# Kernel tuning notes

Hardware: AMD Instinct MI355X
Metric: run time of the kernel (lower is better)

Reference implementation:

```python
import jax, jax.numpy as jnp
import numpy as np
import math

DIM = 768
HEADS = 12
HEAD_DIM = DIM // HEADS
EPS = 1e-6


def rms_norm(x, w):
    return x * jax.lax.rsqrt(jnp.mean(x * x, axis=-1, keepdims=True) + EPS) * w


def rotate_half(x):
    # torch.cat([-x[..., 1::2], x[..., ::2]], dim=-1)
    return jnp.concatenate([-x[..., 1::2], x[..., ::2]], axis=-1)


def setup_inputs() -> dict:
    key = jax.random.key(0)
    ks = jax.random.split(key, 12)
    b, n = 2, 2048
    s = 0.02
    return {
        "x": jax.random.normal(ks[0], (b, n, DIM), jnp.float32),
        "cos": jax.random.uniform(ks[1], (1, 1, n, HEAD_DIM), jnp.float32),
        "sin": jax.random.uniform(ks[2], (1, 1, n, HEAD_DIM), jnp.float32),
        "mask": jnp.zeros((1, 1, n, n), jnp.float32),
        "wq": jax.random.normal(ks[3], (DIM, DIM), jnp.float32) * s,
        "wk": jax.random.normal(ks[4], (DIM, DIM), jnp.float32) * s,
        "wv": jax.random.normal(ks[5], (DIM, DIM), jnp.float32) * s,
        "wo": jax.random.normal(ks[6], (DIM, DIM), jnp.float32) * s,
        "bo": jnp.zeros((DIM,), jnp.float32),
        "g_attn": jnp.ones((DIM,), jnp.float32),
        "g_ffn": jnp.ones((DIM,), jnp.float32),
        "w1": jax.random.normal(ks[7], (DIM, 4 * DIM), jnp.float32) * s,
        "b1": jnp.zeros((4 * DIM,), jnp.float32),
        "w2": jax.random.normal(ks[8], (4 * DIM, DIM), jnp.float32) * s,
        "b2": jnp.zeros((DIM,), jnp.float32),
    }


def reference(x, cos, sin, mask, wq, wk, wv, wo, bo, g_attn, g_ffn, w1, b1, w2, b2):
    b, n, _ = x.shape
    h = rms_norm(x, g_attn)
    # [b, n, dim] -> [b, heads, n, head_dim]
    def split_heads(t):
        return t.reshape(b, n, HEADS, HEAD_DIM).transpose(0, 2, 1, 3)
    q = split_heads(h @ wq)
    k = split_heads(h @ wk)
    v = split_heads(h @ wv)
    q = q * cos + rotate_half(q) * sin
    k = k * cos + rotate_half(k) * sin
    scores = jnp.einsum("bhqd,bhkd->bhqk", q, k) / math.sqrt(HEAD_DIM)
    scores = scores + mask
    attn = jax.nn.softmax(scores, axis=-1)
    out = jnp.einsum("bhqk,bhkd->bhqd", attn, v)
    out = out.transpose(0, 2, 1, 3).reshape(b, n, DIM)
    x = x + (out @ wo + bo)  # dropout is identity in eval
    h2 = rms_norm(x, g_ffn)
    ffn = jax.nn.silu(h2 @ w1 + b1) @ w2 + b2
    return x + ffn
```

## Files before the change

### kernel.cpp

```cpp
#include <hip/hip_runtime.h>
#include <hip/hip_bf16.h>

typedef unsigned short u16;
typedef unsigned int u32;
typedef float f32x4 __attribute__((ext_vector_type(4)));
typedef short bf16x8 __attribute__((ext_vector_type(8)));
typedef int i32x4 __attribute__((ext_vector_type(4)));
typedef unsigned short u16x8 __attribute__((ext_vector_type(8)));

#define DIM 768
#define NTOK 4096
#define NSEQ 2048
#define NHEAD 12
#define HDIM 64

__device__ __forceinline__ u16 f2bf(float f) {
    u32 u = __builtin_bit_cast(u32, f);
    u32 r = (u + 0x7FFFu + ((u >> 16) & 1u)) >> 16;
    return (u16)r;
}
__device__ __forceinline__ float bf2f(u16 h) {
    return __builtin_bit_cast(float, ((u32)h) << 16);
}

__global__ __launch_bounds__(256) void rmsnorm_cast(
    const float* __restrict__ X, const float* __restrict__ g, u16* __restrict__ H)
{
    const int row = blockIdx.x;
    const int tid = threadIdx.x;
    const float* xr = X + (long)row * DIM;
    float v0 = xr[tid], v1 = xr[tid + 256], v2 = xr[tid + 512];
    float ss = v0 * v0 + v1 * v1 + v2 * v2;
    #pragma unroll
    for (int o = 1; o < 64; o <<= 1) ss += __shfl_xor(ss, o);
    __shared__ float wsum[4];
    if ((tid & 63) == 0) wsum[tid >> 6] = ss;
    __syncthreads();
    float tot = wsum[0] + wsum[1] + wsum[2] + wsum[3];
    float sc = rsqrtf(tot * (1.0f / DIM) + 1e-6f);
    u16* hr = H + (long)row * DIM;
    hr[tid]       = f2bf(v0 * sc * g[tid]);
    hr[tid + 256] = f2bf(v1 * sc * g[tid + 256]);
    hr[tid + 512] = f2bf(v2 * sc * g[tid + 512]);
}

__global__ __launch_bounds__(256) void transpose_cvt(
    const float* __restrict__ in, u16* __restrict__ out, int R, int C)
{
    __shared__ float t[64][65];
    const int tid = threadIdx.x;
    const long ct = (long)blockIdx.x * 64, rt = (long)blockIdx.y * 64;
    #pragma unroll
    for (int j = 0; j < 4; ++j) {
        int f = j * 256 + tid;
        int row = f >> 4, c0 = (f & 15) * 4;
        f32x4 v = *(const f32x4*)(in + (rt + row) * C + ct + c0);
        #pragma unroll
        for (int i = 0; i < 4; ++i) t[row][c0 + i] = v[i];
    }
    __syncthreads();
    #pragma unroll
    for (int j = 0; j < 2; ++j) {
        int f = j * 256 + tid;
        int c = f >> 3, r0 = (f & 7) * 8;
        u16x8 o;
        #pragma unroll
        for (int i = 0; i < 8; ++i) o[i] = f2bf(t[r0 + i][c]);
        *(u16x8*)(out + (ct + c) * R + rt + r0) = o;
    }
}

__device__ __forceinline__ void rope_row(const u16* __restrict__ src,
                                         u16* __restrict__ dst,
                                         const float* __restrict__ cs,
                                         const float* __restrict__ sn)
{
    u16x8 qv[8];
    #pragma unroll
    for (int i = 0; i < 8; ++i) qv[i] = ((const u16x8*)src)[i];
    u16x8 ov[8];
    #pragma unroll
    for (int j = 0; j < 32; ++j) {
        float xj  = bf2f(qv[j >> 3][j & 7]);
        float xo  = bf2f(qv[(2 * j + 1) >> 3][(2 * j + 1) & 7]);
        float xhj = bf2f(qv[(32 + j) >> 3][j & 7]);
        float xe  = bf2f(qv[(2 * j) >> 3][(2 * j) & 7]);
        float lo = xj * cs[j] - xo * sn[j];
        float hi = xhj * cs[32 + j] + xe * sn[32 + j];
        ov[j >> 3][j & 7] = f2bf(lo);
        ov[4 + (j >> 3)][j & 7] = f2bf(hi);
    }
    #pragma unroll
    for (int i = 0; i < 8; ++i) ((u16x8*)dst)[i] = ov[i];
}

__global__ __launch_bounds__(256) void rope_qk(
    const u16* __restrict__ QKV, const float* __restrict__ cosT,
    const float* __restrict__ sinT, u16* __restrict__ Qr, u16* __restrict__ Kr)
{
    int gid = blockIdx.x * 256 + threadIdx.x;
    int h = gid % NHEAD, token = gid / NHEAD;
    int b = token >> 11, n = token & 2047;
    const float* cs = cosT + (long)n * HDIM;
    const float* sn = sinT + (long)n * HDIM;
    long dsto = (((long)b * NHEAD + h) * NSEQ + n) * HDIM;
    rope_row(QKV + (long)token * 2304 + h * HDIM,       Qr + dsto, cs, sn);
    rope_row(QKV + (long)token * 2304 + DIM + h * HDIM, Kr + dsto, cs, sn);
}

__global__ __launch_bounds__(256) void v_transpose(
    const u16* __restrict__ QKV, u16* __restrict__ Vt)
{
    __shared__ u32 t[64][65];
    const int tid = threadIdx.x;
    const int nt = blockIdx.x, bh = blockIdx.y;
    const int b = bh / NHEAD, h = bh - b * NHEAD;
    const long tok0 = (long)b * NSEQ + nt * 64;
    #pragma unroll
    for (int j = 0; j < 2; ++j) {
        int f = j * 256 + tid;
        int n = f >> 3, d0 = (f & 7) * 8;
        u16x8 v = *(const u16x8*)(QKV + (tok0 + n) * 2304 + 1536 + h * HDIM + d0);
        #pragma unroll
        for (int i = 0; i < 8; ++i) t[n][d0 + i] = v[i];
    }
    __syncthreads();
    #pragma unroll
    for (int j = 0; j < 2; ++j) {
        int f = j * 256 + tid;
        int d = f >> 3, n0 = (f & 7) * 8;
        u16x8 o;
        #pragma unroll
        for (int i = 0; i < 8; ++i) o[i] = (u16)t[n0 + i][d];
        *(u16x8*)(Vt + ((long)bh * HDIM + d) * NSEQ + nt * 64 + n0) = o;
    }
}

template <int EPI>
__global__ __launch_bounds__(256) void gemm_nt(
    const u16* __restrict__ A, const u16* __restrict__ Bt,
    void* __restrict__ Cp, const float* __restrict__ bias,
    const float* __restrict__ resid, int M, int N, int K, int ldc)
{
    __shared__ __align__(16) char smA[128 * 128];
    __shared__ __align__(16) char smB[128 * 128];
    const int tid = threadIdx.x, lane = tid & 63, wid = tid >> 6;
    const int wr = wid >> 1, wc = wid & 1;
    const long mbase = (long)blockIdx.y * 128, nbase = (long)blockIdx.x * 128;
    const char* Ab = (const char*)A;
    const char* Bb = (const char*)Bt;
    const long strideA = (long)K * 2;

    i32x4 pa[4], pb[4];
    auto loadTile = [&](int kt) {
        long k0b = (long)kt * 128;
        #pragma unroll
        for (int j = 0; j < 4; ++j) {
            int f = (j * 256 + tid) * 16;
            int row = f >> 7, kb = f & 127;
            pa[j] = *(const i32x4*)(Ab + (mbase + row) * strideA + k0b + kb);
            pb[j] = *(const i32x4*)(Bb + (nbase + row) * strideA + k0b + kb);
        }
    };
    auto writeTile = [&]() {
        #pragma unroll
        for (int j = 0; j < 4; ++j) {
            int f = (j * 256 + tid) * 16;
            int row = f >> 7, kb = f & 127;
            int sw = kb ^ ((row & 7) << 4);
            *(i32x4*)(smA + row * 128 + sw) = pa[j];
            *(i32x4*)(smB + row * 128 + sw) = pb[j];
        }
    };

    const f32x4 zero4 = {0.f, 0.f, 0.f, 0.f};
    f32x4 acc[4][4];
    #pragma unroll
    for (int m = 0; m < 4; ++m)
        #pragma unroll
        for (int n = 0; n < 4; ++n) acc[m][n] = zero4;

    const int KT = K >> 6;
    loadTile(0);
    for (int kt = 0; kt < KT; ++kt) {
        __syncthreads();
        writeTile();
        __syncthreads();
        if (kt + 1 < KT) loadTile(kt + 1);
        #pragma unroll
        for (int ks = 0; ks < 2; ++ks) {
            const int kbyte = ks * 64 + ((lane >> 4) << 4);
            bf16x8 af[4], bfr[4];
            #pragma unroll
            for (int m = 0; m < 4; ++m) {
                int row = wr * 64 + m * 16 + (lane & 15);
                af[m] = *(const bf16x8*)(smA + row * 128 + (kbyte ^ ((row & 7) << 4)));
            }
            #pragma unroll
            for (int n = 0; n < 4; ++n) {
                int row = wc * 64 + n * 16 + (lane & 15);
                bfr[n] = *(const bf16x8*)(smB + row * 128 + (kbyte ^ ((row & 7) << 4)));
            }
            #pragma unroll
            for (int m = 0; m < 4; ++m)
                #pragma unroll
                for (int n = 0; n < 4; ++n)
                    acc[m][n] = __builtin_amdgcn_mfma_f32_16x16x32_bf16(
                        af[m], bfr[n], acc[m][n], 0, 0, 0);
        }
    }

    #pragma unroll
    for (int m = 0; m < 4; ++m)
        #pragma unroll
        for (int n = 0; n < 4; ++n)
            #pragma unroll
            for (int r = 0; r < 4; ++r) {
                long row = mbase + wr * 64 + m * 16 + ((lane >> 4) << 2) + r;
                long col = nbase + wc * 64 + n * 16 + (lane & 15);
                long idx = row * ldc + col;
                float v = acc[m][n][r];
                if (EPI == 0) {
                    ((u16*)Cp)[idx] = f2bf(v);
                } else if (EPI == 1) {
                    ((float*)Cp)[idx] = resid[idx] + v + bias[col];
                } else {
                    float t = v + bias[col];
                    ((u16*)Cp)[idx] = f2bf(t / (1.0f + __expf(-t)));
                }
            }
}

__global__ __launch_bounds__(256) void attn_fwd(
    const u16* __restrict__ Qr, const u16* __restrict__ Kr,
    const u16* __restrict__ Vt, u16* __restrict__ AO)
{
    __shared__ __align__(16) char smQ[128 * 128];
    __shared__ __align__(16) char smK[64 * 128];
    __shared__ __align__(16) char smV[64 * 128];
    __shared__ __align__(16) char smP[4 * 32 * 128];
    const int tid = threadIdx.x, lane = tid & 63, wid = tid >> 6;
    const int qt = blockIdx.x, bh = blockIdx.y;
    const char* Qg = (const char*)(Qr + ((long)bh * NSEQ + qt * 128) * HDIM);
    const char* Kg = (const char*)(Kr + (long)bh * NSEQ * HDIM);
    const char* Vg = (const char*)(Vt + (long)bh * HDIM * NSEQ);

    #pragma unroll
    for (int j = 0; j < 4; ++j) {
        int f = (j * 256 + tid) * 16;
        int row = f >> 7, kb = f & 127;
        i32x4 v = *(const i32x4*)(Qg + row * 128 + kb);
        *(i32x4*)(smQ + row * 128 + (kb ^ ((row & 7) << 4))) = v;
    }
    __syncthreads();
    bf16x8 qf[2][2];
    #pragma unroll
    for (int mq = 0; mq < 2; ++mq)
        #pragma unroll
        for (int ks = 0; ks < 2; ++ks) {
            int row = wid * 32 + mq * 16 + (lane & 15);
            int kbyte = ks * 64 + ((lane >> 4) << 4);
            qf[mq][ks] = *(const bf16x8*)(smQ + row * 128 + (kbyte ^ ((row & 7) << 4)));
        }

    const f32x4 zero4 = {0.f, 0.f, 0.f, 0.f};
    f32x4 oacc[2][4];
    float mst[2][4], lst[2][4];
    #pragma unroll
    for (int mq = 0; mq < 2; ++mq) {
        #pragma unroll
        for (int df = 0; df < 4; ++df) oacc[mq][df] = zero4;
        #pragma unroll
        for (int r = 0; r < 4; ++r) { mst[mq][r] = -1e30f; lst[mq][r] = 0.f; }
    }

    i32x4 pk[2], pv[2];
    auto loadKV = [&](int kb) {
        #pragma unroll
        for (int j = 0; j < 2; ++j) {
            int f = (j * 256 + tid) * 16;
            int row = f >> 7, c = f & 127;
            pk[j] = *(const i32x4*)(Kg + ((long)kb * 64 + row) * 128 + c);
            pv[j] = *(const i32x4*)(Vg + (long)row * (NSEQ * 2) + kb * 128 + c);
        }
    };
    loadKV(0);

    for (int kb = 0; kb < 32; ++kb) {
        __syncthreads();
        #pragma unroll
        for (int j = 0; j < 2; ++j) {
            int f = (j * 256 + tid) * 16;
            int row = f >> 7, c = f & 127;
            int sw = c ^ ((row & 7) << 4);
            *(i32x4*)(smK + row * 128 + sw) = pk[j];
            *(i32x4*)(smV + row * 128 + sw) = pv[j];
        }
        __syncthreads();
        if (kb + 1 < 32) loadKV(kb + 1);

        f32x4 s[2][4];
        #pragma unroll
        for (int mq = 0; mq < 2; ++mq)
            #pragma unroll
            for (int n = 0; n < 4; ++n) s[mq][n] = zero4;
        #pragma unroll
        for (int ks = 0; ks < 2; ++ks) {
            int kbyte = ks * 64 + ((lane >> 4) << 4);
            bf16x8 kf[4];
            #pragma unroll
            for (int n = 0; n < 4; ++n) {
                int row = n * 16 + (lane & 15);
                kf[n] = *(const bf16x8*)(smK + row * 128 + (kbyte ^ ((row & 7) << 4)));
            }
            #pragma unroll
            for (int mq = 0; mq < 2; ++mq)
                #pragma unroll
                for (int n = 0; n < 4; ++n)
                    s[mq][n] = __builtin_amdgcn_mfma_f32_16x16x32_bf16(
                        qf[mq][ks], kf[n], s[mq][n], 0, 0, 0);
        }

        #pragma unroll
        for (int mq = 0; mq < 2; ++mq) {
            float rmax[4] = {-1e30f, -1e30f, -1e30f, -1e30f};
            #pragma unroll
            for (int n = 0; n < 4; ++n)
                #pragma unroll
                for (int r = 0; r < 4; ++r) {
                    s[mq][n][r] *= 0.125f;
                    rmax[r] = fmaxf(rmax[r], s[mq][n][r]);
                }
            #pragma unroll
            for (int o = 1; o < 16; o <<= 1)
                #pragma unroll
                for (int r = 0; r < 4; ++r)
                    rmax[r] = fmaxf(rmax[r], __shfl_xor(rmax[r], o));
            float corr[4], rsum[4] = {0.f, 0.f, 0.f, 0.f};
            #pragma unroll
            for (int r = 0; r < 4; ++r) {
                float mnew = fmaxf(mst[mq][r], rmax[r]);
                corr[r] = __expf(mst[mq][r] - mnew);
                mst[mq][r] = mnew;
            }
            #pragma unroll
            for (int n = 0; n < 4; ++n)
                #pragma unroll
                for (int r = 0; r < 4; ++r) {
                    float p = __expf(s[mq][n][r] - mst[mq][r]);
                    s[mq][n][r] = p;
                    rsum[r] += p;
                }
            #pragma unroll
            for (int o = 1; o < 16; o <<= 1)
                #pragma unroll
                for (int r = 0; r < 4; ++r) rsum[r] += __shfl_xor(rsum[r], o);
            #pragma unroll
            for (int r = 0; r < 4; ++r) lst[mq][r] = lst[mq][r] * corr[r] + rsum[r];
            #pragma unroll
            for (int df = 0; df < 4; ++df)
                #pragma unroll
                for (int r = 0; r < 4; ++r) oacc[mq][df][r] *= corr[r];
            #pragma unroll
            for (int n = 0; n < 4; ++n)
                #pragma unroll
                for (int r = 0; r < 4; ++r) {
                    int row = wid * 32 + mq * 16 + ((lane >> 4) << 2) + r;
                    int colb = (n * 16 + (lane & 15)) * 2;
                    *(u16*)(smP + row * 128 + (colb ^ ((row & 7) << 4))) =
                        f2bf(s[mq][n][r]);
                }
        }

        #pragma unroll
        for (int ks = 0; ks < 2; ++ks) {
            int kbyte = ks * 64 + ((lane >> 4) << 4);
            bf16x8 vf[4];
            #pragma unroll
            for (int df = 0; df < 4; ++df) {
                int row = df * 16 + (lane & 15);
                vf[df] = *(const bf16x8*)(smV + row * 128 + (kbyte ^ ((row & 7) << 4)));
            }
            #pragma unroll
            for (int mq = 0; mq < 2; ++mq) {
                int rowp = wid * 32 + mq * 16 + (lane & 15);
                bf16x8 pf = *(const bf16x8*)(smP + rowp * 128 + (kbyte ^ ((rowp & 7) << 4)));
                #pragma unroll
                for (int df = 0; df < 4; ++df)
                    oacc[mq][df] = __builtin_amdgcn_mfma_f32_16x16x32_bf16(
                        pf, vf[df], oacc[mq][df], 0, 0, 0);
            }
        }
    }

    const int b = bh / NHEAD, h = bh - b * NHEAD;
    #pragma unroll
    for (int mq = 0; mq < 2; ++mq)
        #pragma unroll
        for (int df = 0; df < 4; ++df)
            #pragma unroll
            for (int r = 0; r < 4; ++r) {
                long token = (long)b * NSEQ + qt * 128 + wid * 32 + mq * 16 +
                             ((lane >> 4) << 2) + r;
                int col = h * HDIM + df * 16 + (lane & 15);
                AO[token * DIM + col] = f2bf(oacc[mq][df][r] / lst[mq][r]);
            }
}

extern "C" void kernel_launch(void* const* d_in, const int* in_sizes, int n_in,
                              void* d_out, int out_size, void* d_ws, size_t ws_size,
                              hipStream_t stream) {
    const float* x      = (const float*)d_in[0];
    const float* cosT   = (const float*)d_in[1];
    const float* sinT   = (const float*)d_in[2];
    const float* wq     = (const float*)d_in[4];
    const float* wk     = (const float*)d_in[5];
    const float* wv     = (const float*)d_in[6];
    const float* wo     = (const float*)d_in[7];
    const float* bo     = (const float*)d_in[8];
    const float* g_attn = (const float*)d_in[9];
    const float* g_ffn  = (const float*)d_in[10];
    const float* w1     = (const float*)d_in[11];
    const float* b1     = (const float*)d_in[12];
    const float* w2     = (const float*)d_in[13];
    const float* b2     = (const float*)d_in[14];
    float* out = (float*)d_out;
    char* ws = (char*)d_ws;

    constexpr long SZ_H    = (long)NTOK * DIM * 2;
    constexpr long SZ_WQKV = 2304L * DIM * 2;
    constexpr long SZ_WO   = (long)DIM * DIM * 2;
    constexpr long SZ_W1   = 3072L * DIM * 2;
    constexpr long SZ_W2   = (long)DIM * 3072 * 2;
    constexpr long SZ_QKV  = (long)NTOK * 2304 * 2;
    constexpr long SZ_QR   = 24L * NSEQ * HDIM * 2;
    constexpr long SZ_AO   = (long)NTOK * DIM * 2;

    const long OFF_H    = 0;
    const long OFF_WQKV = OFF_H + SZ_H;
    const long OFF_WO   = OFF_WQKV + SZ_WQKV;
    const long OFF_W1   = OFF_WO + SZ_WO;
    const long OFF_W2   = OFF_W1 + SZ_W1;
    const long OFF_QKV  = OFF_W2 + SZ_W2;
    const long OFF_QR   = OFF_QKV + SZ_QKV;
    const long OFF_KR   = OFF_QR + SZ_QR;
    const long OFF_VT   = OFF_KR + SZ_QR;
    const long OFF_AO   = OFF_VT + SZ_QR;
    const long OFF_X2   = OFF_AO + SZ_AO;
    const long OFF_FFN1 = OFF_QKV;

    u16* H     = (u16*)(ws + OFF_H);
    u16* WQKVT = (u16*)(ws + OFF_WQKV);
    u16* WOT   = (u16*)(ws + OFF_WO);
    u16* W1T   = (u16*)(ws + OFF_W1);
    u16* W2T   = (u16*)(ws + OFF_W2);
    u16* QKV   = (u16*)(ws + OFF_QKV);
    u16* QR    = (u16*)(ws + OFF_QR);
    u16* KR    = (u16*)(ws + OFF_KR);
    u16* VT    = (u16*)(ws + OFF_VT);
    u16* AO    = (u16*)(ws + OFF_AO);
    float* X2  = (float*)(ws + OFF_X2);
    u16* FFN1  = (u16*)(ws + OFF_FFN1);

    transpose_cvt<<<dim3(12, 12), 256, 0, stream>>>(wq, WQKVT,                 DIM, DIM);
    transpose_cvt<<<dim3(12, 12), 256, 0, stream>>>(wk, WQKVT + 768L * 768,    DIM, DIM);
    transpose_cvt<<<dim3(12, 12), 256, 0, stream>>>(wv, WQKVT + 2L * 768 * 768, DIM, DIM);
    transpose_cvt<<<dim3(12, 12), 256, 0, stream>>>(wo, WOT, DIM, DIM);
    transpose_cvt<<<dim3(48, 12), 256, 0, stream>>>(w1, W1T, DIM, 3072);
    transpose_cvt<<<dim3(12, 48), 256, 0, stream>>>(w2, W2T, 3072, DIM);

    rmsnorm_cast<<<NTOK, 256, 0, stream>>>(x, g_attn, H);
    gemm_nt<0><<<dim3(18, 32), 256, 0, stream>>>(H, WQKVT, QKV, nullptr, nullptr,
                                                 NTOK, 2304, DIM, 2304);
    rope_qk<<<192, 256, 0, stream>>>(QKV, cosT, sinT, QR, KR);
    v_transpose<<<dim3(32, 24), 256, 0, stream>>>(QKV, VT);
    attn_fwd<<<dim3(16, 24), 256, 0, stream>>>(QR, KR, VT, AO);
    gemm_nt<1><<<dim3(6, 32), 256, 0, stream>>>(AO, WOT, X2, bo, x,
                                                NTOK, DIM, DIM, DIM);

    rmsnorm_cast<<<NTOK, 256, 0, stream>>>(X2, g_ffn, H);
    gemm_nt<2><<<dim3(24, 32), 256, 0, stream>>>(H, W1T, FFN1, b1, nullptr,
                                                 NTOK, 3072, DIM, 3072);
    gemm_nt<1><<<dim3(6, 32), 256, 0, stream>>>(FFN1, W2T, out, b2, X2,
                                                NTOK, DIM, 3072, DIM);
}
```

Measured before the change: 367.0 us.

## Use direct global-to-LDS loads in GEMM and attention, shrink attention query tile

GEMM and attention now stage tiles with global_load_lds, writing straight into shared memory with pre-swizzled source addresses, instead of going through registers. This drops the register prefetch, so the load of the next tile no longer overlaps compute, and each iteration waits on a barrier. Attention blocks now cover 64 queries instead of 128 (one 16-row MFMA tile per wave), which doubles the grid for more parallelism but means K/V is reloaded twice as often. The four 768x768 weight transposes are merged into a single launch.

```diff
diff --git a/kernel.cpp b/kernel.cpp
--- a/kernel.cpp
+++ b/kernel.cpp
@@ -21,6 +21,12 @@
 }
 __device__ __forceinline__ float bf2f(u16 h) {
     return __builtin_bit_cast(float, ((u32)h) << 16);
+}
+
+__device__ __forceinline__ void gload16(const void* g, void* l) {
+    __builtin_amdgcn_global_load_lds(
+        (const __attribute__((address_space(1))) unsigned int*)g,
+        (__attribute__((address_space(3))) unsigned int*)l, 16, 0, 0);
 }
 
 __global__ __launch_bounds__(256) void rmsnorm_cast(
@@ -44,12 +50,12 @@
     hr[tid + 512] = f2bf(v2 * sc * g[tid + 512]);
 }
 
-__global__ __launch_bounds__(256) void transpose_cvt(
-    const float* __restrict__ in, u16* __restrict__ out, int R, int C)
+__device__ __forceinline__ void transpose_cvt_body(
+    const float* __restrict__ in, u16* __restrict__ out, int R, int C,
+    int bx, int by, int tid)
 {
     __shared__ float t[64][65];
-    const int tid = threadIdx.x;
-    const long ct = (long)blockIdx.x * 64, rt = (long)blockIdx.y * 64;
+    const long ct = (long)bx * 64, rt = (long)by * 64;
     #pragma unroll
     for (int j = 0; j < 4; ++j) {
         int f = j * 256 + tid;
@@ -68,6 +74,28 @@
         for (int i = 0; i < 8; ++i) o[i] = f2bf(t[r0 + i][c]);
         *(u16x8*)(out + (ct + c) * R + rt + r0) = o;
     }
+}
+
+__global__ __launch_bounds__(256) void transpose_cvt(
+    const float* __restrict__ in, u16* __restrict__ out, int R, int C)
+{
+    transpose_cvt_body(in, out, R, C, blockIdx.x, blockIdx.y, threadIdx.x);
+}
+
+struct Cvt4Args {
+    const float* in0; const float* in1; const float* in2; const float* in3;
+    u16* out0; u16* out1; u16* out2; u16* out3;
+};
+__global__ __launch_bounds__(256) void transpose_cvt4(Cvt4Args a)
+{
+    const float* in; u16* out;
+    switch (blockIdx.z) {
+        case 0: in = a.in0; out = a.out0; break;
+        case 1: in = a.in1; out = a.out1; break;
+        case 2: in = a.in2; out = a.out2; break;
+        default: in = a.in3; out = a.out3; break;
+    }
+    transpose_cvt_body(in, out, DIM, DIM, blockIdx.x, blockIdx.y, threadIdx.x);
 }
 
 __device__ __forceinline__ void rope_row(const u16* __restrict__ src,
@@ -151,28 +179,6 @@
     const char* Bb = (const char*)Bt;
     const long strideA = (long)K * 2;
 
-    i32x4 pa[4], pb[4];
-    auto loadTile = [&](int kt) {
-        long k0b = (long)kt * 128;
-        #pragma unroll
-        for (int j = 0; j < 4; ++j) {
-            int f = (j * 256 + tid) * 16;
-            int row = f >> 7, kb = f & 127;
-            pa[j] = *(const i32x4*)(Ab + (mbase + row) * strideA + k0b + kb);
-            pb[j] = *(const i32x4*)(Bb + (nbase + row) * strideA + k0b + kb);
-        }
-    };
-    auto writeTile = [&]() {
-        #pragma unroll
-        for (int j = 0; j < 4; ++j) {
-            int f = (j * 256 + tid) * 16;
-            int row = f >> 7, kb = f & 127;
-            int sw = kb ^ ((row & 7) << 4);
-            *(i32x4*)(smA + row * 128 + sw) = pa[j];
-            *(i32x4*)(smB + row * 128 + sw) = pb[j];
-        }
-    };
-
     const f32x4 zero4 = {0.f, 0.f, 0.f, 0.f};
     f32x4 acc[4][4];
     #pragma unroll
@@ -181,12 +187,18 @@
         for (int n = 0; n < 4; ++n) acc[m][n] = zero4;
 
     const int KT = K >> 6;
-    loadTile(0);
     for (int kt = 0; kt < KT; ++kt) {
+        const long k0b = (long)kt * 128;
+        #pragma unroll
+        for (int j = 0; j < 4; ++j) {
+            int flat = (j * 256 + tid) * 16;
+            int row = flat >> 7, c = flat & 127;
+            int csw = c ^ ((row & 7) << 4);
+            int ldst = (j * 256 + (tid & 192)) * 16;
+            gload16(Ab + (mbase + row) * strideA + k0b + csw, smA + ldst);
+            gload16(Bb + (nbase + row) * strideA + k0b + csw, smB + ldst);
+        }
         __syncthreads();
-        writeTile();
-        __syncthreads();
-        if (kt + 1 < KT) loadTile(kt + 1);
         #pragma unroll
         for (int ks = 0; ks < 2; ++ks) {
             const int kbyte = ks * 64 + ((lane >> 4) << 4);
@@ -208,6 +220,7 @@
                     acc[m][n] = __builtin_amdgcn_mfma_f32_16x16x32_bf16(
                         af[m], bfr[n], acc[m][n], 0, 0, 0);
         }
+        __syncthreads();
     }
 
     #pragma unroll
@@ -235,75 +248,55 @@
     const u16* __restrict__ Qr, const u16* __restrict__ Kr,
     const u16* __restrict__ Vt, u16* __restrict__ AO)
 {
-    __shared__ __align__(16) char smQ[128 * 128];
+    __shared__ __align__(16) char smQ[64 * 128];
     __shared__ __align__(16) char smK[64 * 128];
     __shared__ __align__(16) char smV[64 * 128];
-    __shared__ __align__(16) char smP[4 * 32 * 128];
+    __shared__ __align__(16) char smP[64 * 128];
     const int tid = threadIdx.x, lane = tid & 63, wid = tid >> 6;
     const int qt = blockIdx.x, bh = blockIdx.y;
-    const char* Qg = (const char*)(Qr + ((long)bh * NSEQ + qt * 128) * HDIM);
+    const char* Qg = (const char*)(Qr + ((long)bh * NSEQ + qt * 64) * HDIM);
     const char* Kg = (const char*)(Kr + (long)bh * NSEQ * HDIM);
     const char* Vg = (const char*)(Vt + (long)bh * HDIM * NSEQ);
 
     #pragma unroll
-    for (int j = 0; j < 4; ++j) {
-        int f = (j * 256 + tid) * 16;
-        int row = f >> 7, kb = f & 127;
-        i32x4 v = *(const i32x4*)(Qg + row * 128 + kb);
-        *(i32x4*)(smQ + row * 128 + (kb ^ ((row & 7) << 4))) = v;
+    for (int j = 0; j < 2; ++j) {
+        int flat = (j * 256 + tid) * 16;
+        int row = flat >> 7, c = flat & 127;
+        int csw = c ^ ((row & 7) << 4);
+        gload16(Qg + row * 128 + csw, smQ + (j * 256 + (tid & 192)) * 16);
     }
     __syncthreads();
-    bf16x8 qf[2][2];
-    #pragma unroll
-    for (int mq = 0; mq < 2; ++mq)
-        #pragma unroll
-        for (int ks = 0; ks < 2; ++ks) {
-            int row = wid * 32 + mq * 16 + (lane & 15);
-            int kbyte = ks * 64 + ((lane >> 4) << 4);
-            qf[mq][ks] = *(const bf16x8*)(smQ + row * 128 + (kbyte ^ ((row & 7) << 4)));
-        }
+    bf16x8 qf[2];
+    #pragma unroll
+    for (int ks = 0; ks < 2; ++ks) {
+        int row = wid * 16 + (lane & 15);
+        int kbyte = ks * 64 + ((lane >> 4) << 4);
+        qf[ks] = *(const bf16x8*)(smQ + row * 128 + (kbyte ^ ((row & 7) << 4)));
+    }
 
     const f32x4 zero4 = {0.f, 0.f, 0.f, 0.f};
-    f32x4 oacc[2][4];
-    float mst[2][4], lst[2][4];
-    #pragma unroll
-    for (int mq = 0; mq < 2; ++mq) {
-        #pragma unroll
-        for (int df = 0; df < 4; ++df) oacc[mq][df] = zero4;
-        #pragma unroll
-        for (int r = 0; r < 4; ++r) { mst[mq][r] = -1e30f; lst[mq][r] = 0.f; }
-    }
-
-    i32x4 pk[2], pv[2];
-    auto loadKV = [&](int kb) {
+    f32x4 oacc[4];
+    float mst[4], lst[4];
+    #pragma unroll
+    for (int df = 0; df < 4; ++df) oacc[df] = zero4;
+    #pragma unroll
+    for (int r = 0; r < 4; ++r) { mst[r] = -1e30f; lst[r] = 0.f; }
+
+    for (int kb = 0; kb < 32; ++kb) {
         #pragma unroll
         for (int j = 0; j < 2; ++j) {
-            int f = (j * 256 + tid) * 16;
-            int row = f >> 7, c = f & 127;
-            pk[j] = *(const i32x4*)(Kg + ((long)kb * 64 + row) * 128 + c);
-            pv[j] = *(const i32x4*)(Vg + (long)row * (NSEQ * 2) + kb * 128 + c);
-        }
-    };
-    loadKV(0);
-
-    for (int kb = 0; kb < 32; ++kb) {
+            int flat = (j * 256 + tid) * 16;
+            int row = flat >> 7, c = flat & 127;
+            int csw = c ^ ((row & 7) << 4);
+            int ldst = (j * 256 + (tid & 192)) * 16;
+            gload16(Kg + ((long)kb * 64 + row) * 128 + csw, smK + ldst);
+            gload16(Vg + (long)row * (NSEQ * 2) + kb * 128 + csw, smV + ldst);
+        }
         __syncthreads();
-        #pragma unroll
-        for (int j = 0; j < 2; ++j) {
-            int f = (j * 256 + tid) * 16;
-            int row = f >> 7, c = f & 127;
-            int sw = c ^ ((row & 7) << 4);
-            *(i32x4*)(smK + row * 128 + sw) = pk[j];
-            *(i32x4*)(smV + row * 128 + sw) = pv[j];
-        }
-        __syncthreads();
-        if (kb + 1 < 32) loadKV(kb + 1);
-
-        f32x4 s[2][4];
-        #pragma unroll
-        for (int mq = 0; mq < 2; ++mq)
-            #pragma unroll
-            for (int n = 0; n < 4; ++n) s[mq][n] = zero4;
+
+        f32x4 s[4];
+        #pragma unroll
+        for (int n = 0; n < 4; ++n) s[n] = zero4;
         #pragma unroll
         for (int ks = 0; ks < 2; ++ks) {
             int kbyte = ks * 64 + ((lane >> 4) << 4);
@@ -314,63 +307,57 @@
                 kf[n] = *(const bf16x8*)(smK + row * 128 + (kbyte ^ ((row & 7) << 4)));
             }
             #pragma unroll
-            for (int mq = 0; mq < 2; ++mq)
-                #pragma unroll
-                for (int n = 0; n < 4; ++n)
-                    s[mq][n] = __builtin_amdgcn_mfma_f32_16x16x32_bf16(
-                        qf[mq][ks], kf[n], s[mq][n], 0, 0, 0);
-        }
-
-        #pragma unroll
-        for (int mq = 0; mq < 2; ++mq) {
-            float rmax[4] = {-1e30f, -1e30f, -1e30f, -1e30f};
-            #pragma unroll
             for (int n = 0; n < 4; ++n)
-                #pragma unroll
-                for (int r = 0; r < 4; ++r) {
-                    s[mq][n][r] *= 0.125f;
-                    rmax[r] = fmaxf(rmax[r], s[mq][n][r]);
-                }
-            #pragma unroll
-            for (int o = 1; o < 16; o <<= 1)
-                #pragma unroll
-                for (int r = 0; r < 4; ++r)
-                    rmax[r] = fmaxf(rmax[r], __shfl_xor(rmax[r], o));
-            float corr[4], rsum[4] = {0.f, 0.f, 0.f, 0.f};
+                s[n] = __builtin_amdgcn_mfma_f32_16x16x32_bf16(
+                    qf[ks], kf[n], s[n], 0, 0, 0);
+        }
+
+        float rmax[4] = {-1e30f, -1e30f, -1e30f, -1e30f};
+        #pragma unroll
+        for (int n = 0; n < 4; ++n)
             #pragma unroll
             for (int r = 0; r < 4; ++r) {
-                float mnew = fmaxf(mst[mq][r], rmax[r]);
-                corr[r] = __expf(mst[mq][r] - mnew);
-                mst[mq][r] = mnew;
-            }
-            #pragma unroll
-            for (int n = 0; n < 4; ++n)
-                #pragma unroll
-                for (int r = 0; r < 4; ++r) {
-                    float p = __expf(s[mq][n][r] - mst[mq][r]);
-                    s[mq][n][r] = p;
-                    rsum[r] += p;
-                }
-            #pragma unroll
-            for (int o = 1; o < 16; o <<= 1)
-                #pragma unroll
-                for (int r = 0; r < 4; ++r) rsum[r] += __shfl_xor(rsum[r], o);
-            #pragma unroll
-            for (int r = 0; r < 4; ++r) lst[mq][r] = lst[mq][r] * corr[r] + rsum[r];
-            #pragma unroll
-            for (int df = 0; df < 4; ++df)
-                #pragma unroll
-                for (int r = 0; r < 4; ++r) oacc[mq][df][r] *= corr[r];
-            #pragma unroll
-            for (int n = 0; n < 4; ++n)
-                #pragma unroll
-                for (int r = 0; r < 4; ++r) {
-                    int row = wid * 32 + mq * 16 + ((lane >> 4) << 2) + r;
-                    int colb = (n * 16 + (lane & 15)) * 2;
-                    *(u16*)(smP + row * 128 + (colb ^ ((row & 7) << 4))) =
-                        f2bf(s[mq][n][r]);
-                }
-        }
+                s[n][r] *= 0.125f;
+                rmax[r] = fmaxf(rmax[r], s[n][r]);
+            }
+        #pragma unroll
+        for (int o = 1; o < 16; o <<= 1)
+            #pragma unroll
+            for (int r = 0; r < 4; ++r)
+                rmax[r] = fmaxf(rmax[r], __shfl_xor(rmax[r], o));
+        float corr[4], rsum[4] = {0.f, 0.f, 0.f, 0.f};
+        #pragma unroll
+        for (int r = 0; r < 4; ++r) {
+            float mnew = fmaxf(mst[r], rmax[r]);
+            corr[r] = __expf(mst[r] - mnew);
+            mst[r] = mnew;
+        }
+        #pragma unroll
+        for (int n = 0; n < 4; ++n)
+            #pragma unroll
+            for (int r = 0; r < 4; ++r) {
+                float p = __expf(s[n][r] - mst[r]);
+                s[n][r] = p;
+                rsum[r] += p;
+            }
+        #pragma unroll
+        for (int o = 1; o < 16; o <<= 1)
+            #pragma unroll
+            for (int r = 0; r < 4; ++r) rsum[r] += __shfl_xor(rsum[r], o);
+        #pragma unroll
+        for (int r = 0; r < 4; ++r) lst[r] = lst[r] * corr[r] + rsum[r];
+        #pragma unroll
+        for (int df = 0; df < 4; ++df)
+            #pragma unroll
+            for (int r = 0; r < 4; ++r) oacc[df][r] *= corr[r];
+        #pragma unroll
+        for (int n = 0; n < 4; ++n)
+            #pragma unroll
+            for (int r = 0; r < 4; ++r) {
+                int row = wid * 16 + ((lane >> 4) << 2) + r;
+                int colb = (n * 16 + (lane & 15)) * 2;
+                *(u16*)(smP + row * 128 + (colb ^ ((row & 7) << 4))) = f2bf(s[n][r]);
+            }
 
         #pragma unroll
         for (int ks = 0; ks < 2; ++ks) {
@@ -381,30 +368,25 @@
                 int row = df * 16 + (lane & 15);
                 vf[df] = *(const bf16x8*)(smV + row * 128 + (kbyte ^ ((row & 7) << 4)));
             }
-            #pragma unroll
-            for (int mq = 0; mq < 2; ++mq) {
-                int rowp = wid * 32 + mq * 16 + (lane & 15);
-                bf16x8 pf = *(const bf16x8*)(smP + rowp * 128 + (kbyte ^ ((rowp & 7) << 4)));
-                #pragma unroll
-                for (int df = 0; df < 4; ++df)
-                    oacc[mq][df] = __builtin_amdgcn_mfma_f32_16x16x32_bf16(
-                        pf, vf[df], oacc[mq][df], 0, 0, 0);
-            }
-        }
+            int rowp = wid * 16 + (lane & 15);
+            bf16x8 pf = *(const bf16x8*)(smP + rowp * 128 + (kbyte ^ ((rowp & 7) << 4)));
+            #pragma unroll
+            for (int df = 0; df < 4; ++df)
+                oacc[df] = __builtin_amdgcn_mfma_f32_16x16x32_bf16(
+                    pf, vf[df], oacc[df], 0, 0, 0);
+        }
+        __syncthreads();
     }
 
     const int b = bh / NHEAD, h = bh - b * NHEAD;
     #pragma unroll
-    for (int mq = 0; mq < 2; ++mq)
-        #pragma unroll
-        for (int df = 0; df < 4; ++df)
-            #pragma unroll
-            for (int r = 0; r < 4; ++r) {
-                long token = (long)b * NSEQ + qt * 128 + wid * 32 + mq * 16 +
-                             ((lane >> 4) << 2) + r;
-                int col = h * HDIM + df * 16 + (lane & 15);
-                AO[token * DIM + col] = f2bf(oacc[mq][df][r] / lst[mq][r]);
-            }
+    for (int df = 0; df < 4; ++df)
+        #pragma unroll
+        for (int r = 0; r < 4; ++r) {
+            long token = (long)b * NSEQ + qt * 64 + wid * 16 + ((lane >> 4) << 2) + r;
+            int col = h * HDIM + df * 16 + (lane & 15);
+            AO[token * DIM + col] = f2bf(oacc[df][r] / lst[r]);
+        }
 }
 
 extern "C" void kernel_launch(void* const* d_in, const int* in_sizes, int n_in,
@@ -462,10 +444,9 @@
     float* X2  = (float*)(ws + OFF_X2);
     u16* FFN1  = (u16*)(ws + OFF_FFN1);
 
-    transpose_cvt<<<dim3(12, 12), 256, 0, stream>>>(wq, WQKVT,                 DIM, DIM);
-    transpose_cvt<<<dim3(12, 12), 256, 0, stream>>>(wk, WQKVT + 768L * 768,    DIM, DIM);
-    transpose_cvt<<<dim3(12, 12), 256, 0, stream>>>(wv, WQKVT + 2L * 768 * 768, DIM, DIM);
-    transpose_cvt<<<dim3(12, 12), 256, 0, stream>>>(wo, WOT, DIM, DIM);
+    Cvt4Args c4 = { wq, wk, wv, wo,
+                    WQKVT, WQKVT + 768L * 768, WQKVT + 2L * 768 * 768, WOT };
+    transpose_cvt4<<<dim3(12, 12, 4), 256, 0, stream>>>(c4);
     transpose_cvt<<<dim3(48, 12), 256, 0, stream>>>(w1, W1T, DIM, 3072);
     transpose_cvt<<<dim3(12, 48), 256, 0, stream>>>(w2, W2T, 3072, DIM);
 
@@ -474,7 +455,7 @@
                                                  NTOK, 2304, DIM, 2304);
     rope_qk<<<192, 256, 0, stream>>>(QKV, cosT, sinT, QR, KR);
     v_transpose<<<dim3(32, 24), 256, 0, stream>>>(QKV, VT);
-    attn_fwd<<<dim3(16, 24), 256, 0, stream>>>(QR, KR, VT, AO);
+    attn_fwd<<<dim3(32, 24), 256, 0, stream>>>(QR, KR, VT, AO);
     gemm_nt<1><<<dim3(6, 32), 256, 0, stream>>>(AO, WOT, X2, bo, x,
                                                 NTOK, DIM, DIM, DIM);
 
```

Result: no change. 372.5 us (+1.5%).
